# Kernel tuning notes

Measured on AMD Instinct MI355X. Metric: run time of the kernel, lower is better.

## Reference

```python
import jax, jax.numpy as jnp
import numpy as np


def _conv1x1(x, W, b):
    # 1x1 conv == per-pixel channel matmul: x [B,C,H,W], W [O,C], b [O]
    return jnp.einsum('bchw,oc->bohw', x, W) + b[None, :, None, None]


def setup_inputs() -> dict:
    key = jax.random.key(0)
    ks = jax.random.split(key, 9)
    B, C, H, W = 16, 512, 32, 32
    s = 1.0 / np.sqrt(C)
    inp = {
        'x': jax.random.normal(ks[0], (B, C, H, W), dtype=jnp.float32),
        'Wq': jax.random.normal(ks[1], (C, C), dtype=jnp.float32) * s,
        'bq': jax.random.normal(ks[2], (C,), dtype=jnp.float32) * 0.01,
        'Wk': jax.random.normal(ks[3], (C, C), dtype=jnp.float32) * s,
        'bk': jax.random.normal(ks[4], (C,), dtype=jnp.float32) * 0.01,
        'Wv': jax.random.normal(ks[5], (C, C), dtype=jnp.float32) * s,
        'bv': jax.random.normal(ks[6], (C,), dtype=jnp.float32) * 0.01,
        'Wo': jax.random.normal(ks[7], (C, C), dtype=jnp.float32) * s,
        'bo': jax.random.normal(ks[8], (C,), dtype=jnp.float32) * 0.01,
    }
    return inp


def reference(x, Wq, bq, Wk, bk, Wv, bv, Wo, bo):
    B, C, H, W = x.shape
    q = _conv1x1(x, Wq, bq)
    k = _conv1x1(x, Wk, bk)
    v = _conv1x1(x, Wv, bv)
    hw = H * W
    qf = q.reshape(B, C, hw)  # [B,C,HW]
    kf = k.reshape(B, C, hw)
    vf = v.reshape(B, C, hw)
    # scores[b,i,j] = sum_c q[b,c,i] * k[b,c,j], scaled by c^-0.5
    scores = jnp.einsum('bci,bcj->bij', qf, kf) * (C ** -0.5)
    attn = jax.nn.softmax(scores, axis=2)  # softmax over keys j
    # out[b,c,i] = sum_j v[b,c,j] * attn[b,i,j]
    out = jnp.einsum('bcj,bij->bci', vf, attn).reshape(B, C, H, W)
    out = _conv1x1(out, Wo, bo)
    return x + out
```

## Files before the change

### kernel.cpp

```cpp
#include <hip/hip_runtime.h>
#include <hip/hip_bf16.h>
#include <math.h>


typedef __bf16 bf16x8 __attribute__((ext_vector_type(8)));
typedef float  f32x16 __attribute__((ext_vector_type(16)));

__device__ __forceinline__ unsigned short f2bf(float f) {
    unsigned u = __float_as_uint(f);
    u += 0x7fff + ((u >> 16) & 1);
    return (unsigned short)(u >> 16);
}

__device__ __forceinline__ void gload_lds16(const void* g, void* l) {
    __builtin_amdgcn_global_load_lds(
        (const __attribute__((address_space(1))) void*)g,
        (__attribute__((address_space(3))) void*)l, 16, 0, 0);
}

struct GemmP {
    const unsigned short* A;
    const unsigned short* B;
    void* C;
    const float* bias;
    const float* resid;
    float* lsum;
    int M, N, K, ldA, ldB;
    long sA, sB, sC, sR;
    int ln_nn, ln_pb;
    float scale;
};

template<bool OUT_F32, int BIAS_MODE, bool RESID, int EXPM>
__device__ __forceinline__ void gemm_body(const GemmP p, int L,
                                          unsigned short* Als,
                                          unsigned short* Bls)
{
    const int xcd = L & 7;
    const int idx = L >> 3;
    const int bz  = xcd * 2 + (idx >> p.ln_pb);
    const int w   = idx & ((1 << p.ln_pb) - 1);
    const int m0  = (w >> p.ln_nn) << 7;
    const int n0  = (w & ((1 << p.ln_nn) - 1)) << 7;

    const unsigned short* A = p.A + bz * p.sA;
    const unsigned short* B = p.B + bz * p.sB;

    const int tid  = threadIdx.x;
    const int lane = tid & 63;
    const int wave = tid >> 6;
    const int wm   = wave >> 1;
    const int wn   = wave & 1;

    const int ar = lane >> 2;
    const int ak = (((lane & 3) ^ ((ar >> 1) & 3))) * 8;

    const unsigned short* agp = A + (long)(m0 + wave * 16 + ar) * p.ldA + ak;
    const unsigned short* bgp = B + (long)(n0 + wave * 16 + ar) * p.ldB + ak;
    const long aj = 64L * p.ldA;
    const long bj = 64L * p.ldB;

    const int ln31 = lane & 31;
    const int hi   = lane >> 5;
    const int swz  = ((ln31 >> 1) & 3) << 3;
    const int aoff = (wm * 64 + ln31) * 32;
    const int boff = (wn * 64 + ln31) * 32;
    const int koff0 = (hi * 8) ^ swz;
    const int koff1 = (16 + hi * 8) ^ swz;

    f32x16 acc[2][2] = {};

    const int nsteps = p.K >> 5;

    auto STAGE = [&](int sel) {
        unsigned short* a0 = Als + sel * 4096;
        unsigned short* b0 = Bls + sel * 4096;
        gload_lds16(agp,      a0 + wave * 512);
        gload_lds16(agp + aj, a0 + (wave + 4) * 512);
        gload_lds16(bgp,      b0 + wave * 512);
        gload_lds16(bgp + bj, b0 + (wave + 4) * 512);
        agp += 32; bgp += 32;
    };

    auto COMPUTE = [&](int sel) {
        const unsigned short* Ap = Als + sel * 4096;
        const unsigned short* Bp = Bls + sel * 4096;
        bf16x8 af[2][2], bfr[2][2];
        #pragma unroll
        for (int mt = 0; mt < 2; ++mt) {
            af[mt][0] = *(const bf16x8*)&Ap[aoff + mt * 1024 + koff0];
            af[mt][1] = *(const bf16x8*)&Ap[aoff + mt * 1024 + koff1];
        }
        #pragma unroll
        for (int nt = 0; nt < 2; ++nt) {
            bfr[nt][0] = *(const bf16x8*)&Bp[boff + nt * 1024 + koff0];
            bfr[nt][1] = *(const bf16x8*)&Bp[boff + nt * 1024 + koff1];
        }
        #pragma unroll
        for (int ks = 0; ks < 2; ++ks)
            #pragma unroll
            for (int mt = 0; mt < 2; ++mt)
                #pragma unroll
                for (int nt = 0; nt < 2; ++nt)
                    acc[mt][nt] = __builtin_amdgcn_mfma_f32_32x32x16_bf16(
                        af[mt][ks], bfr[nt][ks], acc[mt][nt], 0, 0, 0);
    };

    STAGE(0);
    STAGE(1);

    int bc = 0, bn = 1, bs = 2;
    for (int t = 0; t < nsteps - 1; ++t) {
        __builtin_amdgcn_sched_barrier(0);
        asm volatile("s_waitcnt vmcnt(4)" ::: "memory");
        __builtin_amdgcn_s_barrier();
        asm volatile("" ::: "memory");
        __builtin_amdgcn_sched_barrier(0);
        if (t + 2 < nsteps) STAGE(bs);
        COMPUTE(bc);
        const int tmp = bc; bc = bn; bn = bs; bs = tmp;
    }
    __builtin_amdgcn_sched_barrier(0);
    asm volatile("s_waitcnt vmcnt(0)" ::: "memory");
    __builtin_amdgcn_s_barrier();
    asm volatile("" ::: "memory");
    __builtin_amdgcn_sched_barrier(0);
    COMPUTE(bc);

    float* Cf = (float*)p.C + bz * p.sC;
    unsigned short* Ch = (unsigned short*)p.C + bz * p.sC;
    const float* resid = RESID ? (p.resid + bz * p.sR) : nullptr;
    const int N = p.N;

    if (EXPM == 1) {
        float* lrow = p.lsum + bz * (long)p.M;
        #pragma unroll
        for (int mt = 0; mt < 2; ++mt) {
            #pragma unroll
            for (int r = 0; r < 16; ++r) {
                const int row = m0 + wm * 64 + mt * 32 +
                                (r & 3) + 8 * (r >> 2) + 4 * hi;
                float rs = 0.0f;
                #pragma unroll
                for (int nt = 0; nt < 2; ++nt) {
                    const int col = n0 + wn * 64 + nt * 32 + ln31;
                    const float e = __expf(acc[mt][nt][r] * p.scale);
                    rs += e;
                    Ch[(long)row * N + col] = f2bf(e);
                }
                rs += __shfl_xor(rs, 1);
                rs += __shfl_xor(rs, 2);
                rs += __shfl_xor(rs, 4);
                rs += __shfl_xor(rs, 8);
                rs += __shfl_xor(rs, 16);
                if (ln31 == 0) atomicAdd(&lrow[row], rs);
            }
        }
    } else {
        #pragma unroll
        for (int mt = 0; mt < 2; ++mt) {
            float linv[16];
            if (EXPM == 2) {
                const float* lrow = p.lsum + bz * (long)p.M;
                #pragma unroll
                for (int r = 0; r < 16; ++r)
                    linv[r] = 1.0f / lrow[m0 + wm * 64 + mt * 32 +
                                          (r & 3) + 8 * (r >> 2) + 4 * hi];
            }
            #pragma unroll
            for (int nt = 0; nt < 2; ++nt) {
                const int col = n0 + wn * 64 + nt * 32 + ln31;
                const float bn2 = (BIAS_MODE == 2) ? p.bias[col] : 0.0f;
                #pragma unroll
                for (int r = 0; r < 16; ++r) {
                    const int row = m0 + wm * 64 + mt * 32 +
                                    (r & 3) + 8 * (r >> 2) + 4 * hi;
                    float val = acc[mt][nt][r] + bn2;
                    if (BIAS_MODE == 1) val += p.bias[row];
                    if (EXPM == 2) val *= linv[r];
                    const long o = (long)row * N + col;
                    if (RESID) val += resid[o];
                    if (OUT_F32) Cf[o] = val;
                    else         Ch[o] = f2bf(val);
                }
            }
        }
    }
}

template<bool OUT_F32, int BIAS_MODE, bool RESID, int EXPM>
__global__ __launch_bounds__(256) void gemm_bt_mfma(GemmP p)
{
    __shared__ unsigned short Als[3 * 4096];
    __shared__ unsigned short Bls[3 * 4096];
    gemm_body<OUT_F32, BIAS_MODE, RESID, EXPM>(p, blockIdx.x, Als, Bls);
}

__global__ __launch_bounds__(256) void gemm_qkv_fused(GemmP pqk, GemmP pv, int split)
{
    __shared__ unsigned short Als[3 * 4096];
    __shared__ unsigned short Bls[3 * 4096];
    if ((int)blockIdx.x < split)
        gemm_body<false, 2, false, 0>(pqk, blockIdx.x, Als, Bls);
    else
        gemm_body<false, 1, false, 0>(pv, blockIdx.x - split, Als, Bls);
}

__global__ __launch_bounds__(256) void prep_all(
    const float* __restrict__ x, unsigned short* __restrict__ xT,
    const float* __restrict__ Wq, const float* __restrict__ Wk,
    const float* __restrict__ Wv, const float* __restrict__ Wo,
    const float* __restrict__ bq, const float* __restrict__ bk,
    unsigned short* __restrict__ Wb, float* __restrict__ biasqk,
    float* __restrict__ lsum)
{
    const int b = blockIdx.x;
    const int t = threadIdx.x;
    if (b < 8192) {
        __shared__ float tl[32][33];
        const int batch = b >> 9;
        const int rem = b & 511;
        const int p0 = (rem & 31) * 32;
        const int c0 = (rem >> 5) * 32;
        const float* xb = x + (long)batch * 524288;
        unsigned short* xTb = xT + (long)batch * 524288;
        const int tx = t & 31;
        const int ty = t >> 5;
        #pragma unroll
        for (int i = 0; i < 4; ++i)
            tl[ty + 8 * i][tx] = xb[(long)(c0 + ty + 8 * i) * 1024 + p0 + tx];
        __syncthreads();
        #pragma unroll
        for (int i = 0; i < 4; ++i)
            xTb[(long)(p0 + ty + 8 * i) * 512 + c0 + tx] = f2bf(tl[tx][ty + 8 * i]);
    } else if (b < 9216) {
        const int wb = b - 8192;
        const float* srcs[4] = {Wq, Wk, Wv, Wo};
        const float* s = srcs[wb >> 8];
        unsigned short* d = Wb + (long)(wb >> 8) * 262144;
        const int i = ((wb & 255) * 256 + t) * 4;
        const float4 f = *(const float4*)(s + i);
        ushort4 h;
        h.x = f2bf(f.x); h.y = f2bf(f.y); h.z = f2bf(f.z); h.w = f2bf(f.w);
        *(ushort4*)(d + i) = h;
    } else {
        biasqk[t]       = bq[t];
        biasqk[256 + t] = bq[256 + t];
        biasqk[512 + t] = bk[t];
        biasqk[768 + t] = bk[256 + t];
        #pragma unroll
        for (int i = 0; i < 64; ++i) lsum[i * 256 + t] = 0.0f;
    }
}

extern "C" void kernel_launch(void* const* d_in, const int* in_sizes, int n_in,
                              void* d_out, int out_size, void* d_ws, size_t ws_size,
                              hipStream_t stream)
{
    const float* x  = (const float*)d_in[0];
    const float* Wq = (const float*)d_in[1];
    const float* bq = (const float*)d_in[2];
    const float* Wk = (const float*)d_in[3];
    const float* bk = (const float*)d_in[4];
    const float* Wv = (const float*)d_in[5];
    const float* bv = (const float*)d_in[6];
    const float* Wo = (const float*)d_in[7];
    const float* bo = (const float*)d_in[8];
    float* out = (float*)d_out;

    const int Bn = 16, C = 512, HW = 1024;
    const long CHW = (long)C * HW;
    const long SHW = (long)HW * HW;

    unsigned short* xT   = (unsigned short*)d_ws;
    unsigned short* qkT  = xT + Bn * CHW;
    unsigned short* vB   = qkT + Bn * SHW;
    unsigned short* expS = vB + Bn * CHW;
    unsigned short* Wb   = expS + Bn * SHW;
    float* biasqk = (float*)(Wb + 4 * 262144);
    float* lsum   = biasqk + 1024;
    unsigned short* OT = xT;

    unsigned short* Wvb = Wb + 2 * 262144;
    unsigned short* Wob = Wb + 3 * 262144;

    const dim3 blk(256);
    const float scale = 0.044194173824159216f;

    prep_all<<<dim3(9217), blk, 0, stream>>>(x, xT, Wq, Wk, Wv, Wo, bq, bk,
                                             Wb, biasqk, lsum);

    GemmP pqk = { xT, Wb, qkT, biasqk, nullptr, nullptr,
                  HW, 2 * C, C, C, C, CHW, 0, SHW, 0, 3, 6, 0.0f };
    GemmP pv  = { Wvb, xT, vB, bv, nullptr, nullptr,
                  C, HW, C, C, C, 0, CHW, CHW, 0, 3, 5, 0.0f };
    gemm_qkv_fused<<<dim3(1536), blk, 0, stream>>>(pqk, pv, 1024);

    GemmP ps  = { qkT, qkT + C, expS, nullptr, nullptr, lsum,
                  HW, HW, C, 2 * C, 2 * C, SHW, SHW, SHW, 0, 3, 6, scale };
    gemm_bt_mfma<false, 0, false, 1><<<dim3(1024), blk, 0, stream>>>(ps);

    GemmP po  = { expS, vB, OT, nullptr, nullptr, lsum,
                  HW, C, HW, HW, HW, SHW, CHW, CHW, 0, 2, 5, 0.0f };
    gemm_bt_mfma<false, 0, false, 2><<<dim3(512), blk, 0, stream>>>(po);

    GemmP pout = { Wob, OT, out, bo, x, nullptr,
                   C, HW, C, C, C, 0, CHW, CHW, CHW, 3, 5, 0.0f };
    gemm_bt_mfma<true, 1, true, 0><<<dim3(512), blk, 0, stream>>>(pout);
}
```

Measured before the change: 233.9 us.

## Widen GEMM tiles to 128x256 and compute softmax row sums via MFMA with ones

The block tile grows from 128x128 to 128x256. Each wave now covers all 128 rows and a 64-column slice, which doubles reuse of the A operand and halves the grid sizes. The softmax denominator no longer comes from atomicAdd of row sums in the exp kernel. Instead it is recomputed in the PV GEMM by an extra MFMA of the exp tile against a ones vector, which removes the atomics, the lsum buffer and its zeroing. The change also raises LDS and register use and adds MFMA work in the PV kernel. Fewer blocks may leave some CUs underused.

```diff
diff --git a/kernel.cpp b/kernel.cpp
--- a/kernel.cpp
+++ b/kernel.cpp
@@ -24,7 +24,6 @@
     void* C;
     const float* bias;
     const float* resid;
-    float* lsum;
     int M, N, K, ldA, ldB;
     long sA, sB, sC, sR;
     int ln_nn, ln_pb;
@@ -41,7 +40,7 @@
     const int bz  = xcd * 2 + (idx >> p.ln_pb);
     const int w   = idx & ((1 << p.ln_pb) - 1);
     const int m0  = (w >> p.ln_nn) << 7;
-    const int n0  = (w & ((1 << p.ln_nn) - 1)) << 7;
+    const int n0  = (w & ((1 << p.ln_nn) - 1)) << 8;
 
     const unsigned short* A = p.A + bz * p.sA;
     const unsigned short* B = p.B + bz * p.sB;
@@ -49,8 +48,6 @@
     const int tid  = threadIdx.x;
     const int lane = tid & 63;
     const int wave = tid >> 6;
-    const int wm   = wave >> 1;
-    const int wn   = wave & 1;
 
     const int ar = lane >> 2;
     const int ak = (((lane & 3) ^ ((ar >> 1) & 3))) * 8;
@@ -63,47 +60,57 @@
     const int ln31 = lane & 31;
     const int hi   = lane >> 5;
     const int swz  = ((ln31 >> 1) & 3) << 3;
-    const int aoff = (wm * 64 + ln31) * 32;
-    const int boff = (wn * 64 + ln31) * 32;
     const int koff0 = (hi * 8) ^ swz;
     const int koff1 = (16 + hi * 8) ^ swz;
 
-    f32x16 acc[2][2] = {};
+    f32x16 acc[4][2] = {};
+    f32x16 acc1[4] = {};
+    bf16x8 ones;
+    if constexpr (EXPM == 2) {
+        #pragma unroll
+        for (int i = 0; i < 8; ++i) ones[i] = (__bf16)1.0f;
+    }
 
     const int nsteps = p.K >> 5;
 
     auto STAGE = [&](int sel) {
         unsigned short* a0 = Als + sel * 4096;
-        unsigned short* b0 = Bls + sel * 4096;
-        gload_lds16(agp,      a0 + wave * 512);
-        gload_lds16(agp + aj, a0 + (wave + 4) * 512);
-        gload_lds16(bgp,      b0 + wave * 512);
-        gload_lds16(bgp + bj, b0 + (wave + 4) * 512);
+        unsigned short* b0 = Bls + sel * 8192;
+        gload_lds16(agp,          a0 + wave * 512);
+        gload_lds16(agp + aj,     a0 + (wave + 4) * 512);
+        gload_lds16(bgp,          b0 + wave * 512);
+        gload_lds16(bgp + bj,     b0 + (wave + 4) * 512);
+        gload_lds16(bgp + 2 * bj, b0 + (wave + 8) * 512);
+        gload_lds16(bgp + 3 * bj, b0 + (wave + 12) * 512);
         agp += 32; bgp += 32;
     };
 
     auto COMPUTE = [&](int sel) {
         const unsigned short* Ap = Als + sel * 4096;
-        const unsigned short* Bp = Bls + sel * 4096;
-        bf16x8 af[2][2], bfr[2][2];
-        #pragma unroll
-        for (int mt = 0; mt < 2; ++mt) {
-            af[mt][0] = *(const bf16x8*)&Ap[aoff + mt * 1024 + koff0];
-            af[mt][1] = *(const bf16x8*)&Ap[aoff + mt * 1024 + koff1];
-        }
-        #pragma unroll
-        for (int nt = 0; nt < 2; ++nt) {
-            bfr[nt][0] = *(const bf16x8*)&Bp[boff + nt * 1024 + koff0];
-            bfr[nt][1] = *(const bf16x8*)&Bp[boff + nt * 1024 + koff1];
-        }
-        #pragma unroll
-        for (int ks = 0; ks < 2; ++ks)
-            #pragma unroll
-            for (int mt = 0; mt < 2; ++mt)
+        const unsigned short* Bp = Bls + sel * 8192;
+        #pragma unroll
+        for (int ks = 0; ks < 2; ++ks) {
+            const int ko = ks ? koff1 : koff0;
+            bf16x8 af[4], bfr[2];
+            #pragma unroll
+            for (int mt = 0; mt < 4; ++mt)
+                af[mt] = *(const bf16x8*)&Ap[(mt * 32 + ln31) * 32 + ko];
+            #pragma unroll
+            for (int nt = 0; nt < 2; ++nt)
+                bfr[nt] = *(const bf16x8*)&Bp[(wave * 64 + nt * 32 + ln31) * 32 + ko];
+            if constexpr (EXPM == 2) {
+                #pragma unroll
+                for (int mt = 0; mt < 4; ++mt)
+                    acc1[mt] = __builtin_amdgcn_mfma_f32_32x32x16_bf16(
+                        af[mt], ones, acc1[mt], 0, 0, 0);
+            }
+            #pragma unroll
+            for (int mt = 0; mt < 4; ++mt)
                 #pragma unroll
                 for (int nt = 0; nt < 2; ++nt)
                     acc[mt][nt] = __builtin_amdgcn_mfma_f32_32x32x16_bf16(
-                        af[mt][ks], bfr[nt][ks], acc[mt][nt], 0, 0, 0);
+                        af[mt], bfr[nt], acc[mt][nt], 0, 0, 0);
+        }
     };
 
     STAGE(0);
@@ -112,7 +119,7 @@
     int bc = 0, bn = 1, bs = 2;
     for (int t = 0; t < nsteps - 1; ++t) {
         __builtin_amdgcn_sched_barrier(0);
-        asm volatile("s_waitcnt vmcnt(4)" ::: "memory");
+        asm volatile("s_waitcnt vmcnt(6)" ::: "memory");
         __builtin_amdgcn_s_barrier();
         asm volatile("" ::: "memory");
         __builtin_amdgcn_sched_barrier(0);
@@ -132,74 +139,46 @@
     const float* resid = RESID ? (p.resid + bz * p.sR) : nullptr;
     const int N = p.N;
 
-    if (EXPM == 1) {
-        float* lrow = p.lsum + bz * (long)p.M;
-        #pragma unroll
-        for (int mt = 0; mt < 2; ++mt) {
-            #pragma unroll
-            for (int r = 0; r < 16; ++r) {
-                const int row = m0 + wm * 64 + mt * 32 +
-                                (r & 3) + 8 * (r >> 2) + 4 * hi;
-                float rs = 0.0f;
-                #pragma unroll
-                for (int nt = 0; nt < 2; ++nt) {
-                    const int col = n0 + wn * 64 + nt * 32 + ln31;
-                    const float e = __expf(acc[mt][nt][r] * p.scale);
-                    rs += e;
-                    Ch[(long)row * N + col] = f2bf(e);
+    #pragma unroll
+    for (int mt = 0; mt < 4; ++mt) {
+        #pragma unroll
+        for (int r = 0; r < 16; ++r) {
+            const int row = m0 + mt * 32 + (r & 3) + 8 * (r >> 2) + 4 * hi;
+            float rv = 0.0f;
+            if constexpr (EXPM == 2) rv = 1.0f / acc1[mt][r];
+            const float bm = (BIAS_MODE == 1) ? p.bias[row] : 0.0f;
+            #pragma unroll
+            for (int nt = 0; nt < 2; ++nt) {
+                const int col = n0 + wave * 64 + nt * 32 + ln31;
+                float val = acc[mt][nt][r];
+                if constexpr (EXPM == 1) {
+                    val = __expf(val * p.scale);
+                } else {
+                    if (BIAS_MODE == 1) val += bm;
+                    if (BIAS_MODE == 2) val += p.bias[col];
+                    if constexpr (EXPM == 2) val *= rv;
                 }
-                rs += __shfl_xor(rs, 1);
-                rs += __shfl_xor(rs, 2);
-                rs += __shfl_xor(rs, 4);
-                rs += __shfl_xor(rs, 8);
-                rs += __shfl_xor(rs, 16);
-                if (ln31 == 0) atomicAdd(&lrow[row], rs);
+                const long o = (long)row * N + col;
+                if (RESID) val += resid[o];
+                if (OUT_F32) Cf[o] = val;
+                else         Ch[o] = f2bf(val);
             }
         }
-    } else {
-        #pragma unroll
-        for (int mt = 0; mt < 2; ++mt) {
-            float linv[16];
-            if (EXPM == 2) {
-                const float* lrow = p.lsum + bz * (long)p.M;
-                #pragma unroll
-                for (int r = 0; r < 16; ++r)
-                    linv[r] = 1.0f / lrow[m0 + wm * 64 + mt * 32 +
-                                          (r & 3) + 8 * (r >> 2) + 4 * hi];
-            }
-            #pragma unroll
-            for (int nt = 0; nt < 2; ++nt) {
-                const int col = n0 + wn * 64 + nt * 32 + ln31;
-                const float bn2 = (BIAS_MODE == 2) ? p.bias[col] : 0.0f;
-                #pragma unroll
-                for (int r = 0; r < 16; ++r) {
-                    const int row = m0 + wm * 64 + mt * 32 +
-                                    (r & 3) + 8 * (r >> 2) + 4 * hi;
-                    float val = acc[mt][nt][r] + bn2;
-                    if (BIAS_MODE == 1) val += p.bias[row];
-                    if (EXPM == 2) val *= linv[r];
-                    const long o = (long)row * N + col;
-                    if (RESID) val += resid[o];
-                    if (OUT_F32) Cf[o] = val;
-                    else         Ch[o] = f2bf(val);
-                }
-            }
-        }
     }
 }
 
 template<bool OUT_F32, int BIAS_MODE, bool RESID, int EXPM>
-__global__ __launch_bounds__(256) void gemm_bt_mfma(GemmP p)
+__global__ __launch_bounds__(256, 2) void gemm_bt_mfma(GemmP p)
 {
     __shared__ unsigned short Als[3 * 4096];
-    __shared__ unsigned short Bls[3 * 4096];
+    __shared__ unsigned short Bls[3 * 8192];
     gemm_body<OUT_F32, BIAS_MODE, RESID, EXPM>(p, blockIdx.x, Als, Bls);
 }
 
-__global__ __launch_bounds__(256) void gemm_qkv_fused(GemmP pqk, GemmP pv, int split)
+__global__ __launch_bounds__(256, 2) void gemm_qkv_fused(GemmP pqk, GemmP pv, int split)
 {
     __shared__ unsigned short Als[3 * 4096];
-    __shared__ unsigned short Bls[3 * 4096];
+    __shared__ unsigned short Bls[3 * 8192];
     if ((int)blockIdx.x < split)
         gemm_body<false, 2, false, 0>(pqk, blockIdx.x, Als, Bls);
     else
@@ -211,8 +190,7 @@
     const float* __restrict__ Wq, const float* __restrict__ Wk,
     const float* __restrict__ Wv, const float* __restrict__ Wo,
     const float* __restrict__ bq, const float* __restrict__ bk,
-    unsigned short* __restrict__ Wb, float* __restrict__ biasqk,
-    float* __restrict__ lsum)
+    unsigned short* __restrict__ Wb, float* __restrict__ biasqk)
 {
     const int b = blockIdx.x;
     const int t = threadIdx.x;
@@ -248,8 +226,6 @@
         biasqk[256 + t] = bq[256 + t];
         biasqk[512 + t] = bk[t];
         biasqk[768 + t] = bk[256 + t];
-        #pragma unroll
-        for (int i = 0; i < 64; ++i) lsum[i * 256 + t] = 0.0f;
     }
 }
 
@@ -278,7 +254,6 @@
     unsigned short* expS = vB + Bn * CHW;
     unsigned short* Wb   = expS + Bn * SHW;
     float* biasqk = (float*)(Wb + 4 * 262144);
-    float* lsum   = biasqk + 1024;
     unsigned short* OT = xT;
 
     unsigned short* Wvb = Wb + 2 * 262144;
@@ -288,23 +263,23 @@
     const float scale = 0.044194173824159216f;
 
     prep_all<<<dim3(9217), blk, 0, stream>>>(x, xT, Wq, Wk, Wv, Wo, bq, bk,
-                                             Wb, biasqk, lsum);
-
-    GemmP pqk = { xT, Wb, qkT, biasqk, nullptr, nullptr,
-                  HW, 2 * C, C, C, C, CHW, 0, SHW, 0, 3, 6, 0.0f };
-    GemmP pv  = { Wvb, xT, vB, bv, nullptr, nullptr,
-                  C, HW, C, C, C, 0, CHW, CHW, 0, 3, 5, 0.0f };
-    gemm_qkv_fused<<<dim3(1536), blk, 0, stream>>>(pqk, pv, 1024);
-
-    GemmP ps  = { qkT, qkT + C, expS, nullptr, nullptr, lsum,
-                  HW, HW, C, 2 * C, 2 * C, SHW, SHW, SHW, 0, 3, 6, scale };
-    gemm_bt_mfma<false, 0, false, 1><<<dim3(1024), blk, 0, stream>>>(ps);
-
-    GemmP po  = { expS, vB, OT, nullptr, nullptr, lsum,
-                  HW, C, HW, HW, HW, SHW, CHW, CHW, 0, 2, 5, 0.0f };
-    gemm_bt_mfma<false, 0, false, 2><<<dim3(512), blk, 0, stream>>>(po);
-
-    GemmP pout = { Wob, OT, out, bo, x, nullptr,
-                   C, HW, C, C, C, 0, CHW, CHW, CHW, 3, 5, 0.0f };
-    gemm_bt_mfma<true, 1, true, 0><<<dim3(512), blk, 0, stream>>>(pout);
-}
+                                             Wb, biasqk);
+
+    GemmP pqk = { xT, Wb, qkT, biasqk, nullptr,
+                  HW, 2 * C, C, C, C, CHW, 0, SHW, 0, 2, 5, 0.0f };
+    GemmP pv  = { Wvb, xT, vB, bv, nullptr,
+                  C, HW, C, C, C, 0, CHW, CHW, 0, 2, 4, 0.0f };
+    gemm_qkv_fused<<<dim3(768), blk, 0, stream>>>(pqk, pv, 512);
+
+    GemmP ps  = { qkT, qkT + C, expS, nullptr, nullptr,
+                  HW, HW, C, 2 * C, 2 * C, SHW, SHW, SHW, 0, 2, 5, scale };
+    gemm_bt_mfma<false, 0, false, 1><<<dim3(512), blk, 0, stream>>>(ps);
+
+    GemmP po  = { expS, vB, OT, nullptr, nullptr,
+                  HW, C, HW, HW, HW, SHW, CHW, CHW, 0, 1, 4, 0.0f };
+    gemm_bt_mfma<false, 0, false, 2><<<dim3(256), blk, 0, stream>>>(po);
+
+    GemmP pout = { Wob, OT, out, bo, x,
+                   C, HW, C, C, C, 0, CHW, CHW, CHW, 2, 4, 0.0f };
+    gemm_bt_mfma<true, 1, true, 0><<<dim3(256), blk, 0, stream>>>(pout);
+}
```

After: 249.8 us. +6.8%, slower.
